# Kernel optimization log

Measured on AMD Instinct MI355X. Metric: run time of the kernel, lower is better.

Reference implementation:

```python
import jax, jax.numpy as jnp
import numpy as np

T_, B_, DIM, NB, D, H_, W_ = 4, 4, 256, 16, 16, 32, 32
VTH_L1_LOW = VTH_L1_HIGH = 0.5
EPS = 1e-5

# ---- surrogate-gradient spike (ATan surrogate, alpha=2.0, spikingjelly default) ----
@jax.custom_vjp
def spike(x):
    return (x >= 0).astype(x.dtype)

def _spk_fwd(x):
    return spike(x), x

def _spk_bwd(x, g):
    a = 2.0
    return (g * (a / 2.0) / (1.0 + (jnp.pi / 2.0 * a * x) ** 2),)

spike.defvjp(_spk_fwd, _spk_bwd)

def lif(x, tau=2.0, vth=1.0):
    # MultiStepLIFNode: v += (x - v)/tau; fire at vth; hard reset (detach_reset)
    def step(v, xt):
        v = v + (xt - v) / tau
        s = spike(v - vth)
        v = v * (1.0 - jax.lax.stop_gradient(s))
        return v, s
    _, s = jax.lax.scan(step, jnp.zeros_like(x[0]), x)
    return s

def haar_mat(n):
    m = np.zeros((n, n), np.float32)
    s = 1.0 / np.sqrt(2.0)
    for i in range(n // 2):
        m[i, 2 * i] = s; m[i, 2 * i + 1] = s          # low-pass rows
        m[n // 2 + i, 2 * i] = s; m[n // 2 + i, 2 * i + 1] = -s  # high-pass rows
    return jnp.asarray(m)

def bn(x, g, b):  # training-mode BatchNorm2d over (N,C,H,W)
    mu = jnp.mean(x, axis=(0, 2, 3), keepdims=True)
    var = jnp.var(x, axis=(0, 2, 3), keepdims=True)
    return g.reshape(1, -1, 1, 1) * (x - mu) * jax.lax.rsqrt(var + EPS) + b.reshape(1, -1, 1, 1)

def conv(x, w, b):
    y = jax.lax.conv_general_dilated(x, w, (1, 1), 'SAME',
                                     dimension_numbers=('NCHW', 'OIHW', 'NCHW'))
    return y + b.reshape(1, -1, 1, 1)

def band_gate(c, vth, tau):
    # coefficient spiking threshold then channel-energy sparsity gate
    c = c * spike(jnp.abs(c) - vth)
    E = jnp.mean(c * c, axis=(-2, -1), keepdims=True)  # per (T,B,C) energy
    return c * (E > tau).astype(c.dtype)

def _forward(x, haar_weight, conv1_w, conv1_b, conv2_w, conv2_b,
             bn_fwd_g, bn_fwd_b, bn_mul_g, bn_mul_b, bn_inv_g, bn_inv_b,
             bn_c1_g, bn_c1_b, bn_c2_g, bn_c2_b):
    T, B, C, H, W = x.shape
    HmW, HmH = haar_mat(W), haar_mat(H)
    Hh, Wh, TB = H // 2, W // 2, T * B
    s = lif(x)
    # ---- level-1 Haar along W ----
    y = jnp.einsum('vw,tbchw->tbchv', HmW, s)
    low, high = y[..., :Wh], y[..., Wh:]
    low = low * spike(jnp.abs(low) - VTH_L1_LOW)
    high = high * spike(jnp.abs(high) - VTH_L1_HIGH)
    l1 = jnp.concatenate([low, high], axis=2)  # (T,B,2C,H,Wh)
    l1 = bn(l1.reshape(TB, 2 * C, H, Wh), bn_fwd_g, bn_fwd_b).reshape(T, B, 2 * C, H, Wh)
    # ---- level-2 Haar along H + per-band sparsity ----
    lo, hi = l1[:, :, :C], l1[:, :, C:]
    zlo = jnp.einsum('vh,tbchw->tbcvw', HmH, lo)
    zhi = jnp.einsum('vh,tbchw->tbcvw', HmH, hi)
    LL = band_gate(zlo[..., :Hh, :], 0.5, 0.01)
    HL = band_gate(zlo[..., Hh:, :], 0.5, 0.02)
    LH = band_gate(zhi[..., :Hh, :], 0.5, 0.02)
    HH = band_gate(zhi[..., Hh:, :], 0.5, 0.05)
    l2 = jnp.concatenate([LL, HL, LH, HH], axis=2)  # (T,B,4C,Hh,Wh)
    l2 = bn(l2.reshape(TB, 4 * C, Hh, Wh), bn_mul_g, bn_mul_b)
    # ---- block-diagonal multiply ----
    h = l2.reshape(TB, NB, 4 * D, Hh, Wh).transpose(0, 3, 4, 1, 2)  # (TB,Hh,Wh,NB,4D)
    parts = [jnp.einsum('thwbd,bdk->thwbk', h[..., i * D:(i + 1) * D], haar_weight)
             for i in range(4)]
    h = jnp.concatenate(parts, axis=-1)
    h = h.reshape(TB, Hh, Wh, 4 * C).transpose(0, 3, 1, 2).reshape(T, B, 4 * C, Hh, Wh)
    # ---- inverse Haar ----
    LLc, HLc, LHc, HHc = h[:, :, :C], h[:, :, C:2 * C], h[:, :, 2 * C:3 * C], h[:, :, 3 * C:]
    lo = jnp.einsum('vh,tbcvw->tbchw', HmH, jnp.concatenate([LLc, HLc], axis=-2))
    hi = jnp.einsum('vh,tbcvw->tbchw', HmH, jnp.concatenate([LHc, HHc], axis=-2))
    rec = jnp.einsum('vw,tbchv->tbchw', HmW, jnp.concatenate([lo, hi], axis=-1))
    rec = bn(rec.reshape(TB, C, H, W), bn_inv_g, bn_inv_b).reshape(T, B, C, H, W)
    # ---- conv residual paths over block channels ----
    xr = s.reshape(TB * NB, D, H, W)
    c1 = bn(conv(xr, conv1_w, conv1_b).reshape(TB, C, H, W), bn_c1_g, bn_c1_b).reshape(T, B, C, H, W)
    c2 = bn(conv(xr, conv2_w, conv2_b).reshape(TB, C, H, W), bn_c2_g, bn_c2_b).reshape(T, B, C, H, W)
    return rec + c1 + c2

def setup_inputs() -> dict:
    key = jax.random.key(0)
    ks = jax.random.split(key, 4)
    return {
        'x': jax.random.normal(ks[0], (T_, B_, DIM, H_, W_), jnp.float32),
        'haar_weight': 0.02 * jax.random.normal(ks[1], (NB, D, D), jnp.float32),
        'conv1_w': 0.1 * jax.random.normal(ks[2], (D, D, 1, 1), jnp.float32),
        'conv1_b': jnp.zeros((D,), jnp.float32),
        'conv2_w': 0.05 * jax.random.normal(ks[3], (D, D, 3, 3), jnp.float32),
        'conv2_b': jnp.zeros((D,), jnp.float32),
        'bn_fwd_g': jnp.ones((2 * DIM,), jnp.float32), 'bn_fwd_b': jnp.zeros((2 * DIM,), jnp.float32),
        'bn_mul_g': jnp.ones((4 * DIM,), jnp.float32), 'bn_mul_b': jnp.zeros((4 * DIM,), jnp.float32),
        'bn_inv_g': jnp.ones((DIM,), jnp.float32), 'bn_inv_b': jnp.zeros((DIM,), jnp.float32),
        'bn_c1_g': jnp.ones((DIM,), jnp.float32), 'bn_c1_b': jnp.zeros((DIM,), jnp.float32),
        'bn_c2_g': jnp.ones((DIM,), jnp.float32), 'bn_c2_b': jnp.zeros((DIM,), jnp.float32),
    }

def reference(x, haar_weight, conv1_w, conv1_b, conv2_w, conv2_b,
              bn_fwd_g, bn_fwd_b, bn_mul_g, bn_mul_b, bn_inv_g, bn_inv_b,
              bn_c1_g, bn_c1_b, bn_c2_g, bn_c2_b):
    return _forward(x, haar_weight, conv1_w, conv1_b, conv2_w, conv2_b,
                    bn_fwd_g, bn_fwd_b, bn_mul_g, bn_mul_b, bn_inv_g, bn_inv_b,
                    bn_c1_g, bn_c1_b, bn_c2_g, bn_c2_b)
```

## Files before the change

### kernel.cpp

```cpp
#include <hip/hip_runtime.h>
#include <hip/hip_bf16.h>

#define T_ 4
#define B_ 4
#define C_ 256
#define H_ 32
#define W_ 32
#define TB_ 16
#define Hh_ 16
#define Wh_ 16
#define INVS2 0.70710678118654752440f
#define EPSBN 1e-5f

#define OFF_HW   0
#define OFF_W1   4096
#define OFF_B1   4352
#define OFF_W2   4368
#define OFF_B2   6672
#define OFF_G1   6688
#define OFF_BE1  7200
#define OFF_G2   7712
#define OFF_BE2  8736
#define OFF_G3   9760
#define OFF_BE3  10016
#define OFF_G4   10272
#define OFF_BE4  10528
#define OFF_G5   10784
#define OFF_BE5  11040
#define W_TOTAL  11296
#define NSUMS    4608

struct WPtrs { const void* p[15]; };

typedef __attribute__((ext_vector_type(8))) short short8;
typedef __attribute__((ext_vector_type(4))) float f32x4;

__device__ inline float bf2f(__hip_bfloat16 v) { return __bfloat162float(v); }
__device__ inline float bfu(unsigned short u) { return __uint_as_float((unsigned)u << 16); }

__global__ __launch_bounds__(256) void k_prep(const unsigned short* __restrict__ xr,
                                              WPtrs wp,
                                              __hip_bfloat16* __restrict__ wc,
                                              float* __restrict__ sums,
                                              int* __restrict__ flag) {
    int tid = threadIdx.x;
    int cnt = 0;
    for (int i = tid; i < 2048; i += 256) {
        int e = (xr[i] >> 7) & 0xFF;
        if (e >= 134) cnt++;
    }
    for (int o = 1; o < 64; o <<= 1) cnt += __shfl_xor(cnt, o, 64);
    __shared__ int sh[4];
    if ((tid & 63) == 0) sh[tid >> 6] = cnt;
    __syncthreads();
    int f = (sh[0] + sh[1] + sh[2] + sh[3] >= 32) ? 1 : 0;
    if (blockIdx.x == 0 && tid == 0) *flag = f;

    const int sizes[15] = {4096, 256, 16, 2304, 16, 512, 512, 1024, 1024,
                           256, 256, 256, 256, 256, 256};
    int i = blockIdx.x * 256 + tid;
    if (i < W_TOTAL) {
        int seg = 0, off = 0;
        while (i >= off + sizes[seg]) { off += sizes[seg]; seg++; }
        int j = i - off;
        float v = f ? ((const float*)wp.p[seg])[j]
                    : bf2f(((const __hip_bfloat16*)wp.p[seg])[j]);
        wc[i] = __float2bfloat16(v);
    }
    if (i < NSUMS) sums[i] = 0.f;
}

__global__ __launch_bounds__(256) void k_lifhaar(const void* __restrict__ x_,
                                                 const int* __restrict__ flag,
                                                 unsigned char* __restrict__ s,
                                                 float* __restrict__ sums1) {
    int bid = blockIdx.x;
    int tid = threadIdx.x;
    int half = bid & 1;
    int c = (bid >> 1) & 255;
    int b = bid >> 9;
    int wp = tid & 15;
    int hl = tid >> 4;
    int h = half * 16 + hl;
    int f = *flag;
    const float* xf = (const float*)x_;
    const unsigned int* xb = (const unsigned int*)x_;
    int n = ((b * 256 + c) * 32 + h) * 32 + 2 * wp;

    float v0 = 0.f, v1 = 0.f;
    float aL = 0.f, qL = 0.f, aH = 0.f, qH = 0.f;
    #pragma unroll
    for (int t = 0; t < T_; ++t) {
        size_t idx = (size_t)t * 1048576 + n;
        float x0, x1;
        if (f) {
            float2 xx = *(const float2*)(xf + idx);
            x0 = xx.x; x1 = xx.y;
        } else {
            unsigned int u = xb[idx >> 1];
            x0 = __uint_as_float(u << 16);
            x1 = __uint_as_float(u & 0xffff0000u);
        }
        v0 += (x0 - v0) * 0.5f;
        v1 += (x1 - v1) * 0.5f;
        float s0 = (v0 >= 1.f) ? 1.f : 0.f;
        float s1 = (v1 >= 1.f) ? 1.f : 0.f;
        v0 *= (1.f - s0);
        v1 *= (1.f - s1);
        int tb = t * 4 + b;
        ((uchar2*)s)[(size_t)(tb * 256 + c) * 512 + h * 16 + wp] =
            make_uchar2((unsigned char)s0, (unsigned char)s1);
        float cl = s0 + s1, ch = s0 - s1;
        aL += cl; qL += cl * cl; aH += ch; qH += ch * ch;
    }
    for (int o = 1; o < 64; o <<= 1) {
        aL += __shfl_xor(aL, o, 64); qL += __shfl_xor(qL, o, 64);
        aH += __shfl_xor(aH, o, 64); qH += __shfl_xor(qH, o, 64);
    }
    __shared__ float part[4][4];
    int lane = tid & 63, wv = tid >> 6;
    if (lane == 0) {
        part[wv][0] = aL; part[wv][1] = qL; part[wv][2] = aH; part[wv][3] = qH;
    }
    __syncthreads();
    if (tid < 4) {
        float tot = part[0][tid] + part[1][tid] + part[2][tid] + part[3][tid];
        const int offs[4] = {0, 512, 256, 768};
        atomicAdd(&sums1[offs[tid] + c], tot);
    }
}

__global__ __launch_bounds__(256) void k_stage2(const unsigned char* __restrict__ s,
                                                const float* __restrict__ sums1,
                                                const __hip_bfloat16* __restrict__ wc,
                                                float* __restrict__ stats,
                                                __hip_bfloat16* __restrict__ l2) {
    int blk = blockIdx.x;
    int c = blk & 255;
    int tb = blk >> 8;
    int tid = threadIdx.x;
    int lane = tid & 63, wv = tid >> 6;

    const float nrm = 1.f / 8192.f;
    float mL = sums1[c] * INVS2 * nrm;
    float vL = fmaxf(sums1[512 + c] * 0.5f * nrm - mL * mL, 0.f);
    float sL = bf2f(wc[OFF_G1 + c]) * rsqrtf(vL + EPSBN);
    float tL = bf2f(wc[OFF_BE1 + c]) - mL * sL;
    float mH = sums1[256 + c] * INVS2 * nrm;
    float vH = fmaxf(sums1[768 + c] * 0.5f * nrm - mH * mH, 0.f);
    float sH = bf2f(wc[OFF_G1 + 256 + c]) * rsqrtf(vH + EPSBN);
    float tH = bf2f(wc[OFF_BE1 + 256 + c]) - mH * sH;
    float slo = sL * INVS2, shi = sH * INVS2;

    int w = tid & 15, v = tid >> 4;
    const uchar2* sp = (const uchar2*)(s + ((size_t)(tb * 256 + c)) * 1024);
    uchar2 pa = sp[(2 * v) * 16 + w];
    uchar2 pb = sp[(2 * v + 1) * 16 + w];
    float lt = (float)(pa.x + pa.y) * slo + tL;
    float lb = (float)(pb.x + pb.y) * slo + tL;
    float ht = (float)((int)pa.x - (int)pa.y) * shi + tH;
    float hb = (float)((int)pb.x - (int)pb.y) * shi + tH;

    float zLL = (lt + lb) * INVS2;
    float zHL = (lt - lb) * INVS2;
    float zLH = (ht + hb) * INVS2;
    float zHH = (ht - hb) * INVS2;
    zLL = (fabsf(zLL) - 0.5f >= 0.f) ? zLL : 0.f;
    zHL = (fabsf(zHL) - 0.5f >= 0.f) ? zHL : 0.f;
    zLH = (fabsf(zLH) - 0.5f >= 0.f) ? zLH : 0.f;
    zHH = (fabsf(zHH) - 0.5f >= 0.f) ? zHH : 0.f;

    float r0 = zLL, r1 = zHL, r2 = zLH, r3 = zHH;
    float q0 = zLL * zLL, q1 = zHL * zHL, q2 = zLH * zLH, q3 = zHH * zHH;
    for (int o = 1; o < 64; o <<= 1) {
        r0 += __shfl_xor(r0, o, 64); r1 += __shfl_xor(r1, o, 64);
        r2 += __shfl_xor(r2, o, 64); r3 += __shfl_xor(r3, o, 64);
        q0 += __shfl_xor(q0, o, 64); q1 += __shfl_xor(q1, o, 64);
        q2 += __shfl_xor(q2, o, 64); q3 += __shfl_xor(q3, o, 64);
    }
    __shared__ float part[4][8];
    if (lane == 0) {
        part[wv][0] = r0; part[wv][1] = r1; part[wv][2] = r2; part[wv][3] = r3;
        part[wv][4] = q0; part[wv][5] = q1; part[wv][6] = q2; part[wv][7] = q3;
    }
    __syncthreads();
    float S0 = part[0][0] + part[1][0] + part[2][0] + part[3][0];
    float S1 = part[0][1] + part[1][1] + part[2][1] + part[3][1];
    float S2 = part[0][2] + part[1][2] + part[2][2] + part[3][2];
    float S3 = part[0][3] + part[1][3] + part[2][3] + part[3][3];
    float Q0 = part[0][4] + part[1][4] + part[2][4] + part[3][4];
    float Q1 = part[0][5] + part[1][5] + part[2][5] + part[3][5];
    float Q2 = part[0][6] + part[1][6] + part[2][6] + part[3][6];
    float Q3 = part[0][7] + part[1][7] + part[2][7] + part[3][7];
    float fLL = (Q0 * (1.f / 256.f) > 0.01f) ? 1.f : 0.f;
    float fHL = (Q1 * (1.f / 256.f) > 0.02f) ? 1.f : 0.f;
    float fLH = (Q2 * (1.f / 256.f) > 0.02f) ? 1.f : 0.f;
    float fHH = (Q3 * (1.f / 256.f) > 0.05f) ? 1.f : 0.f;

    float* sums2 = stats + 1024;
    if (tid < 8) {
        const int cho[8] = {0, 1024, 256, 1280, 512, 1536, 768, 1792};
        const float vals[8] = {fLL * S0, fLL * Q0, fHL * S1, fHL * Q1,
                               fLH * S2, fLH * Q2, fHH * S3, fHH * Q3};
        atomicAdd(&sums2[cho[tid] + c], vals[tid]);
    }

    size_t ob = (((size_t)tb * 1024) + c) * 256 + tid;
    l2[ob]               = __float2bfloat16(zLL * fLL);
    l2[ob + 256u * 256u] = __float2bfloat16(zHL * fHL);
    l2[ob + 512u * 256u] = __float2bfloat16(zLH * fLH);
    l2[ob + 768u * 256u] = __float2bfloat16(zHH * fHH);
}

struct SharedU {
    union {
        struct {
            short lo[1025 * 8];
            short hi[1025 * 8];
            unsigned short w2s[2304];
            unsigned short w1s[256];
            unsigned short bs[32];
            float parts[4][4][16];
        } cv;
        struct {
            float wt[4][16][16];
            float bsc[64], bsh[64];
            float parts2[4][32];
        } mi;
    };
};

__global__ __launch_bounds__(256) void k_convmix(const unsigned char* __restrict__ s,
                                                 const __hip_bfloat16* __restrict__ l2,
                                                 const __hip_bfloat16* __restrict__ wc,
                                                 float* __restrict__ stats,
                                                 __hip_bfloat16* __restrict__ rec,
                                                 __hip_bfloat16* __restrict__ c1,
                                                 __hip_bfloat16* __restrict__ c2) {
    __shared__ SharedU sm;
    int bid = blockIdx.x;
    int tid = threadIdx.x;
    int lane = tid & 63, wv = tid >> 6;

    if (bid < 256) {
        int img = bid;
        const unsigned short* wr = (const unsigned short*)wc;
        for (int i = tid; i < 2304; i += 256) sm.cv.w2s[i] = wr[OFF_W2 + i];
        sm.cv.w1s[tid] = wr[OFF_W1 + tid];
        if (tid < 16) { sm.cv.bs[tid] = wr[OFF_B1 + tid]; sm.cv.bs[16 + tid] = wr[OFF_B2 + tid]; }
        if (tid < 8) {
            ((unsigned int*)sm.cv.lo)[4096 + (tid & 3)] = 0;
            ((unsigned int*)sm.cv.hi)[4096 + (tid & 3)] = 0;
        }
        {
            const unsigned int* sp = (const unsigned int*)(s + (size_t)img * 16384);
            int d2 = tid >> 5;
            int pg = tid & 31;
            unsigned int* dst = (unsigned int*)((d2 < 4) ? sm.cv.lo : sm.cv.hi);
            int dl = d2 & 3;
            #pragma unroll
            for (int p = 0; p < 8; ++p) {
                int base = p * 32 + pg;
                unsigned int u0 = sp[d2 * 512 + base];
                unsigned int u1 = sp[d2 * 512 + 256 + base];
                #pragma unroll
                for (int jj = 0; jj < 4; ++jj) {
                    int j = (jj + pg) & 3;
                    unsigned int b0 = (u0 >> (8 * j)) & 255u;
                    unsigned int b1 = (u1 >> (8 * j)) & 255u;
                    unsigned int val = (b0 ? 0x3F80u : 0u) | ((b1 ? 0x3F80u : 0u) << 16);
                    int pix = p * 128 + pg * 4 + j;
                    dst[pix * 4 + dl] = val;
                }
            }
        }
        __syncthreads();

        int m = lane & 15;
        int g = lane >> 4;
        const int tapA[5] = {0, 2, 4, 6, 8};
        const int tapB[5] = {1, 3, 5, 7, 8};

        short8 afr[5], a1f;
        #pragma unroll
        for (int p = 0; p < 5; ++p) {
            int tap = (g < 2) ? tapA[p] : tapB[p];
            short8 av;
            #pragma unroll
            for (int j = 0; j < 8; ++j) {
                int d = (g & 1) * 8 + j;
                unsigned short w = sm.cv.w2s[m * 144 + d * 9 + tap];
                if (p == 4 && g >= 2) w = 0;
                av[j] = (short)w;
            }
            afr[p] = av;
        }
        #pragma unroll
        for (int j = 0; j < 8; ++j) {
            int d = (g & 1) * 8 + j;
            a1f[j] = (g < 2) ? (short)sm.cv.w1s[m * 16 + d] : (short)0;
        }
        float bias1[4], bias2[4];
        #pragma unroll
        for (int r = 0; r < 4; ++r) {
            bias1[r] = bfu(sm.cv.bs[g * 4 + r]);
            bias2[r] = bfu(sm.cv.bs[16 + g * 4 + r]);
        }

        __hip_bfloat16* o1 = c1 + (size_t)img * 16384;
        __hip_bfloat16* o2 = c2 + (size_t)img * 16384;
        const short* bsrc = (g & 1) ? sm.cv.hi : sm.cv.lo;

        float cs1[4] = {0, 0, 0, 0}, cq1[4] = {0, 0, 0, 0};
        float cs2[4] = {0, 0, 0, 0}, cq2[4] = {0, 0, 0, 0};

        for (int t = wv * 16; t < wv * 16 + 16; ++t) {
            int h = t >> 1;
            int w0 = (t & 1) << 4;
            f32x4 acc2 = {0.f, 0.f, 0.f, 0.f};
            f32x4 acc1 = {0.f, 0.f, 0.f, 0.f};
            #pragma unroll
            for (int p = 0; p < 5; ++p) {
                int tap = (g < 2) ? tapA[p] : tapB[p];
                int row = h + tap / 3 - 1;
                int col = w0 + m + (tap % 3) - 1;
                bool ok = ((unsigned)row < 32u) && ((unsigned)col < 32u);
                int idx = ok ? (row * 32 + col) : 1024;
                short8 bv = *(const short8*)&bsrc[idx * 8];
                acc2 = __builtin_amdgcn_mfma_f32_16x16x32_bf16(afr[p], bv, acc2, 0, 0, 0);
                if (p == 2)
                    acc1 = __builtin_amdgcn_mfma_f32_16x16x32_bf16(a1f, bv, acc1, 0, 0, 0);
            }
            int pix = h * 32 + w0 + m;
            #pragma unroll
            for (int r = 0; r < 4; ++r) {
                int k = g * 4 + r;
                float y1 = acc1[r] + bias1[r];
                float y2 = acc2[r] + bias2[r];
                o1[(size_t)k * 1024 + pix] = __float2bfloat16(y1);
                o2[(size_t)k * 1024 + pix] = __float2bfloat16(y2);
                cs1[r] += y1; cq1[r] += y1 * y1;
                cs2[r] += y2; cq2[r] += y2 * y2;
            }
        }
        #pragma unroll
        for (int o = 1; o < 16; o <<= 1) {
            #pragma unroll
            for (int r = 0; r < 4; ++r) {
                cs1[r] += __shfl_xor(cs1[r], o, 64);
                cq1[r] += __shfl_xor(cq1[r], o, 64);
                cs2[r] += __shfl_xor(cs2[r], o, 64);
                cq2[r] += __shfl_xor(cq2[r], o, 64);
            }
        }
        if (m == 0) {
            #pragma unroll
            for (int r = 0; r < 4; ++r) {
                sm.cv.parts[wv][g][r * 4 + 0] = cs1[r];
                sm.cv.parts[wv][g][r * 4 + 1] = cq1[r];
                sm.cv.parts[wv][g][r * 4 + 2] = cs2[r];
                sm.cv.parts[wv][g][r * 4 + 3] = cq2[r];
            }
        }
        __syncthreads();
        if (tid < 64) {
            int gg = tid >> 4, r = (tid >> 2) & 3, which = tid & 3;
            float tot = sm.cv.parts[0][gg][r * 4 + which] + sm.cv.parts[1][gg][r * 4 + which]
                      + sm.cv.parts[2][gg][r * 4 + which] + sm.cv.parts[3][gg][r * 4 + which];
            int ch = (img & 15) * 16 + gg * 4 + r;
            const int base[4] = {3584, 3840, 4096, 4352};
            atomicAdd(&stats[base[which] + ch], tot);
        }
    } else {
        int mb = bid - 256;
        int cg = mb & 15;
        int tb = mb >> 4;
        const float* sums2 = stats + 1024;

        for (int i = tid; i < 1024; i += 256) {
            int q = i >> 8, rem = i & 255, d = rem >> 4, k = rem & 15;
            int nb = q * 4 + (cg >> 2);
            sm.mi.wt[q][d][k] = bf2f(wc[OFF_HW + nb * 256 + d * 16 + k]);
        }
        if (tid < 64) {
            int q = tid >> 4, d = tid & 15;
            int ch = q * 256 + cg * 16 + d;
            float m = sums2[ch] * (1.f / 4096.f);
            float var = fmaxf(sums2[1024 + ch] * (1.f / 4096.f) - m * m, 0.f);
            float sc = bf2f(wc[OFF_G2 + ch]) * rsqrtf(var + EPSBN);
            sm.mi.bsc[tid] = sc;
            sm.mi.bsh[tid] = bf2f(wc[OFF_BE2 + ch]) - m * sc;
        }
        __syncthreads();

        float h[4][16];
        #pragma unroll
        for (int q = 0; q < 4; ++q)
            #pragma unroll
            for (int k = 0; k < 16; ++k) h[q][k] = 0.f;

        int p = tid;
        #pragma unroll
        for (int q = 0; q < 4; ++q) {
            const __hip_bfloat16* base =
                l2 + ((size_t)tb * 1024 + q * 256 + cg * 16) * 256 + p;
            #pragma unroll
            for (int d = 0; d < 16; ++d) {
                float xv = bf2f(base[d * 256]) * sm.mi.bsc[q * 16 + d] + sm.mi.bsh[q * 16 + d];
                #pragma unroll
                for (int k = 0; k < 16; ++k)
                    h[q][k] = fmaf(xv, sm.mi.wt[q][d][k], h[q][k]);
            }
        }

        int uh = tid >> 4, uw = tid & 15;
        __hip_bfloat16* ob = rec + ((size_t)tb * 256 + cg * 16) * 1024;
        float sk[16], qk[16];
        #pragma unroll
        for (int k = 0; k < 16; ++k) {
            float LL = h[0][k], HL = h[1][k], LH = h[2][k], HH = h[3][k];
            float v00 = 0.5f * (LL + HL + LH + HH);
            float v01 = 0.5f * (LL + HL - LH - HH);
            float v10 = 0.5f * (LL - HL + LH - HH);
            float v11 = 0.5f * (LL - HL - LH + HH);
            __hip_bfloat162 top, bot;
            top.x = __float2bfloat16(v00); top.y = __float2bfloat16(v01);
            bot.x = __float2bfloat16(v10); bot.y = __float2bfloat16(v11);
            *(__hip_bfloat162*)(ob + (size_t)k * 1024 + (2 * uh) * 32 + 2 * uw) = top;
            *(__hip_bfloat162*)(ob + (size_t)k * 1024 + (2 * uh + 1) * 32 + 2 * uw) = bot;
            sk[k] = v00 + v01 + v10 + v11;
            qk[k] = v00 * v00 + v01 * v01 + v10 * v10 + v11 * v11;
        }
        for (int o = 1; o < 64; o <<= 1) {
            #pragma unroll
            for (int k = 0; k < 16; ++k) {
                sk[k] += __shfl_xor(sk[k], o, 64);
                qk[k] += __shfl_xor(qk[k], o, 64);
            }
        }
        if (lane == 0) {
            #pragma unroll
            for (int k = 0; k < 16; ++k) {
                sm.mi.parts2[wv][k * 2]     = sk[k];
                sm.mi.parts2[wv][k * 2 + 1] = qk[k];
            }
        }
        __syncthreads();
        if (tid < 32) {
            int k = tid >> 1, which = tid & 1;
            float tot = sm.mi.parts2[0][tid] + sm.mi.parts2[1][tid]
                      + sm.mi.parts2[2][tid] + sm.mi.parts2[3][tid];
            atomicAdd(&stats[3072 + which * 256 + cg * 16 + k], tot);
        }
    }
}

__global__ __launch_bounds__(256) void k_final(const __hip_bfloat16* __restrict__ rec,
                                               const __hip_bfloat16* __restrict__ c1,
                                               const __hip_bfloat16* __restrict__ c2,
                                               const float* __restrict__ stats,
                                               const __hip_bfloat16* __restrict__ wc,
                                               const int* __restrict__ flag,
                                               void* __restrict__ out_) {
    int n8 = blockIdx.x * 256 + threadIdx.x;
    int c = ((n8 * 8) >> 10) & 255;
    const float inv = 1.f / 16384.f;
    float m3 = stats[3072 + c] * inv;
    float v3 = fmaxf(stats[3328 + c] * inv - m3 * m3, 0.f);
    float sc3 = bf2f(wc[OFF_G3 + c]) * rsqrtf(v3 + EPSBN);
    float sh3 = bf2f(wc[OFF_BE3 + c]) - m3 * sc3;
    float m4 = stats[3584 + c] * inv;
    float v4 = fmaxf(stats[3840 + c] * inv - m4 * m4, 0.f);
    float sc4 = bf2f(wc[OFF_G4 + c]) * rsqrtf(v4 + EPSBN);
    float sh4 = bf2f(wc[OFF_BE4 + c]) - m4 * sc4;
    float m5 = stats[4096 + c] * inv;
    float v5 = fmaxf(stats[4352 + c] * inv - m5 * m5, 0.f);
    float sc5 = bf2f(wc[OFF_G5 + c]) * rsqrtf(v5 + EPSBN);
    float sh5 = bf2f(wc[OFF_BE5 + c]) - m5 * sc5;

    short8 r = ((const short8*)rec)[n8];
    short8 a = ((const short8*)c1)[n8];
    short8 b = ((const short8*)c2)[n8];
    float v[8];
    #pragma unroll
    for (int j = 0; j < 8; ++j) {
        v[j] = bfu((unsigned short)r[j]) * sc3 + sh3
             + bfu((unsigned short)a[j]) * sc4 + sh4
             + bfu((unsigned short)b[j]) * sc5 + sh5;
    }
    if (*flag) {
        float4* o = (float4*)out_;
        o[n8 * 2]     = make_float4(v[0], v[1], v[2], v[3]);
        o[n8 * 2 + 1] = make_float4(v[4], v[5], v[6], v[7]);
    } else {
        short8 o;
        #pragma unroll
        for (int j = 0; j < 8; ++j)
            o[j] = (short)__bfloat16_as_ushort(__float2bfloat16(v[j]));
        ((short8*)out_)[n8] = o;
    }
}

extern "C" void kernel_launch(void* const* d_in, const int* in_sizes, int n_in,
                              void* d_out, int out_size, void* d_ws, size_t ws_size,
                              hipStream_t stream) {
    char* ws = (char*)d_ws;
    unsigned char* s_u8  = (unsigned char*)ws;
    __hip_bfloat16* l2   = (__hip_bfloat16*)(ws + ((size_t)8 << 20));
    __hip_bfloat16* rec  = (__hip_bfloat16*)(ws + ((size_t)16 << 20));
    __hip_bfloat16* c1   = (__hip_bfloat16*)(ws + ((size_t)24 << 20));
    __hip_bfloat16* c2   = (__hip_bfloat16*)(ws + ((size_t)32 << 20));
    __hip_bfloat16* wc   = (__hip_bfloat16*)(ws + ((size_t)40 << 20));
    float* stats         = (float*)(ws + ((size_t)40 << 20) + (64 << 10));
    int* flag            = (int*)(ws + ((size_t)40 << 20) + (128 << 10));

    WPtrs wp;
    for (int i = 0; i < 15; ++i) wp.p[i] = d_in[i + 1];

    dim3 blk(256);
    k_prep<<<dim3(45), blk, 0, stream>>>((const unsigned short*)d_in[0], wp, wc, stats, flag);
    k_lifhaar<<<dim3(2048), blk, 0, stream>>>(d_in[0], flag, s_u8, stats);
    k_stage2<<<dim3(4096), blk, 0, stream>>>(s_u8, stats, wc, stats, l2);
    k_convmix<<<dim3(512), blk, 0, stream>>>(s_u8, l2, wc, stats, rec, c1, c2);
    k_final<<<dim3(2048), blk, 0, stream>>>(rec, c1, c2, stats, wc, flag, d_out);
}
```

Before: 150.8 us.

## Fuse four stage kernels into one persistent kernel with software grid barriers

Merges the LIF/Haar, stage-2 band gating, conv-mix and final BN-sum kernels into one 512-block persistent kernel. Phases are separated by an atomic-counter grid barrier with hierarchical counters, and the per-block work from the old larger grids is folded into loops. This removes the launch gaps and tail effects between kernels. In exchange it requires all 512 blocks to be co-resident (launch_bounds 256,2), serializes work per block, and adds spin-wait barrier overhead.

Measured after the change: 302.4 us. 2.01x slower.

```diff
diff --git a/kernel.cpp b/kernel.cpp
--- a/kernel.cpp
+++ b/kernel.cpp
@@ -11,6 +11,7 @@
 #define Wh_ 16
 #define INVS2 0.70710678118654752440f
 #define EPSBN 1e-5f
+#define NBLK 512
 
 #define OFF_HW   0
 #define OFF_W1   4096
@@ -38,10 +39,11 @@
 __device__ inline float bf2f(__hip_bfloat16 v) { return __bfloat162float(v); }
 __device__ inline float bfu(unsigned short u) { return __uint_as_float((unsigned)u << 16); }
 
-__global__ __launch_bounds__(256) void k_prep(const unsigned short* __restrict__ xr,
+__global__ __launch_bounds__(256) void k_init(const unsigned short* __restrict__ xr,
                                               WPtrs wp,
                                               __hip_bfloat16* __restrict__ wc,
                                               float* __restrict__ sums,
+                                              int* __restrict__ bar,
                                               int* __restrict__ flag) {
     int tid = threadIdx.x;
     int cnt = 0;
@@ -68,151 +70,25 @@
         wc[i] = __float2bfloat16(v);
     }
     if (i < NSUMS) sums[i] = 0.f;
+    if (i < 16) bar[i] = 0;
 }
 
-__global__ __launch_bounds__(256) void k_lifhaar(const void* __restrict__ x_,
-                                                 const int* __restrict__ flag,
-                                                 unsigned char* __restrict__ s,
-                                                 float* __restrict__ sums1) {
-    int bid = blockIdx.x;
-    int tid = threadIdx.x;
-    int half = bid & 1;
-    int c = (bid >> 1) & 255;
-    int b = bid >> 9;
-    int wp = tid & 15;
-    int hl = tid >> 4;
-    int h = half * 16 + hl;
-    int f = *flag;
-    const float* xf = (const float*)x_;
-    const unsigned int* xb = (const unsigned int*)x_;
-    int n = ((b * 256 + c) * 32 + h) * 32 + 2 * wp;
-
-    float v0 = 0.f, v1 = 0.f;
-    float aL = 0.f, qL = 0.f, aH = 0.f, qH = 0.f;
-    #pragma unroll
-    for (int t = 0; t < T_; ++t) {
-        size_t idx = (size_t)t * 1048576 + n;
-        float x0, x1;
-        if (f) {
-            float2 xx = *(const float2*)(xf + idx);
-            x0 = xx.x; x1 = xx.y;
-        } else {
-            unsigned int u = xb[idx >> 1];
-            x0 = __uint_as_float(u << 16);
-            x1 = __uint_as_float(u & 0xffff0000u);
-        }
-        v0 += (x0 - v0) * 0.5f;
-        v1 += (x1 - v1) * 0.5f;
-        float s0 = (v0 >= 1.f) ? 1.f : 0.f;
-        float s1 = (v1 >= 1.f) ? 1.f : 0.f;
-        v0 *= (1.f - s0);
-        v1 *= (1.f - s1);
-        int tb = t * 4 + b;
-        ((uchar2*)s)[(size_t)(tb * 256 + c) * 512 + h * 16 + wp] =
-            make_uchar2((unsigned char)s0, (unsigned char)s1);
-        float cl = s0 + s1, ch = s0 - s1;
-        aL += cl; qL += cl * cl; aH += ch; qH += ch * ch;
-    }
-    for (int o = 1; o < 64; o <<= 1) {
-        aL += __shfl_xor(aL, o, 64); qL += __shfl_xor(qL, o, 64);
-        aH += __shfl_xor(aH, o, 64); qH += __shfl_xor(qH, o, 64);
-    }
-    __shared__ float part[4][4];
-    int lane = tid & 63, wv = tid >> 6;
-    if (lane == 0) {
-        part[wv][0] = aL; part[wv][1] = qL; part[wv][2] = aH; part[wv][3] = qH;
-    }
+__device__ __forceinline__ void gbar(int* bs, int phase) {
     __syncthreads();
-    if (tid < 4) {
-        float tot = part[0][tid] + part[1][tid] + part[2][tid] + part[3][tid];
-        const int offs[4] = {0, 512, 256, 768};
-        atomicAdd(&sums1[offs[tid] + c], tot);
-    }
+    if (threadIdx.x == 0) {
+        __threadfence();
+        int t = atomicAdd(&bs[2 + (blockIdx.x & 7)], 1) + 1;
+        if (t == phase * (NBLK / 8)) {
+            int m = atomicAdd(&bs[1], 1) + 1;
+            if (m == phase * 8) atomicAdd(&bs[0], 1);
+        }
+        while (atomicAdd(&bs[0], 0) < phase) __builtin_amdgcn_s_sleep(2);
+        __threadfence();
+    }
+    __syncthreads();
 }
 
-__global__ __launch_bounds__(256) void k_stage2(const unsigned char* __restrict__ s,
-                                                const float* __restrict__ sums1,
-                                                const __hip_bfloat16* __restrict__ wc,
-                                                float* __restrict__ stats,
-                                                __hip_bfloat16* __restrict__ l2) {
-    int blk = blockIdx.x;
-    int c = blk & 255;
-    int tb = blk >> 8;
-    int tid = threadIdx.x;
-    int lane = tid & 63, wv = tid >> 6;
-
-    const float nrm = 1.f / 8192.f;
-    float mL = sums1[c] * INVS2 * nrm;
-    float vL = fmaxf(sums1[512 + c] * 0.5f * nrm - mL * mL, 0.f);
-    float sL = bf2f(wc[OFF_G1 + c]) * rsqrtf(vL + EPSBN);
-    float tL = bf2f(wc[OFF_BE1 + c]) - mL * sL;
-    float mH = sums1[256 + c] * INVS2 * nrm;
-    float vH = fmaxf(sums1[768 + c] * 0.5f * nrm - mH * mH, 0.f);
-    float sH = bf2f(wc[OFF_G1 + 256 + c]) * rsqrtf(vH + EPSBN);
-    float tH = bf2f(wc[OFF_BE1 + 256 + c]) - mH * sH;
-    float slo = sL * INVS2, shi = sH * INVS2;
-
-    int w = tid & 15, v = tid >> 4;
-    const uchar2* sp = (const uchar2*)(s + ((size_t)(tb * 256 + c)) * 1024);
-    uchar2 pa = sp[(2 * v) * 16 + w];
-    uchar2 pb = sp[(2 * v + 1) * 16 + w];
-    float lt = (float)(pa.x + pa.y) * slo + tL;
-    float lb = (float)(pb.x + pb.y) * slo + tL;
-    float ht = (float)((int)pa.x - (int)pa.y) * shi + tH;
-    float hb = (float)((int)pb.x - (int)pb.y) * shi + tH;
-
-    float zLL = (lt + lb) * INVS2;
-    float zHL = (lt - lb) * INVS2;
-    float zLH = (ht + hb) * INVS2;
-    float zHH = (ht - hb) * INVS2;
-    zLL = (fabsf(zLL) - 0.5f >= 0.f) ? zLL : 0.f;
-    zHL = (fabsf(zHL) - 0.5f >= 0.f) ? zHL : 0.f;
-    zLH = (fabsf(zLH) - 0.5f >= 0.f) ? zLH : 0.f;
-    zHH = (fabsf(zHH) - 0.5f >= 0.f) ? zHH : 0.f;
-
-    float r0 = zLL, r1 = zHL, r2 = zLH, r3 = zHH;
-    float q0 = zLL * zLL, q1 = zHL * zHL, q2 = zLH * zLH, q3 = zHH * zHH;
-    for (int o = 1; o < 64; o <<= 1) {
-        r0 += __shfl_xor(r0, o, 64); r1 += __shfl_xor(r1, o, 64);
-        r2 += __shfl_xor(r2, o, 64); r3 += __shfl_xor(r3, o, 64);
-        q0 += __shfl_xor(q0, o, 64); q1 += __shfl_xor(q1, o, 64);
-        q2 += __shfl_xor(q2, o, 64); q3 += __shfl_xor(q3, o, 64);
-    }
-    __shared__ float part[4][8];
-    if (lane == 0) {
-        part[wv][0] = r0; part[wv][1] = r1; part[wv][2] = r2; part[wv][3] = r3;
-        part[wv][4] = q0; part[wv][5] = q1; part[wv][6] = q2; part[wv][7] = q3;
-    }
-    __syncthreads();
-    float S0 = part[0][0] + part[1][0] + part[2][0] + part[3][0];
-    float S1 = part[0][1] + part[1][1] + part[2][1] + part[3][1];
-    float S2 = part[0][2] + part[1][2] + part[2][2] + part[3][2];
-    float S3 = part[0][3] + part[1][3] + part[2][3] + part[3][3];
-    float Q0 = part[0][4] + part[1][4] + part[2][4] + part[3][4];
-    float Q1 = part[0][5] + part[1][5] + part[2][5] + part[3][5];
-    float Q2 = part[0][6] + part[1][6] + part[2][6] + part[3][6];
-    float Q3 = part[0][7] + part[1][7] + part[2][7] + part[3][7];
-    float fLL = (Q0 * (1.f / 256.f) > 0.01f) ? 1.f : 0.f;
-    float fHL = (Q1 * (1.f / 256.f) > 0.02f) ? 1.f : 0.f;
-    float fLH = (Q2 * (1.f / 256.f) > 0.02f) ? 1.f : 0.f;
-    float fHH = (Q3 * (1.f / 256.f) > 0.05f) ? 1.f : 0.f;
-
-    float* sums2 = stats + 1024;
-    if (tid < 8) {
-        const int cho[8] = {0, 1024, 256, 1280, 512, 1536, 768, 1792};
-        const float vals[8] = {fLL * S0, fLL * Q0, fHL * S1, fHL * Q1,
-                               fLH * S2, fLH * Q2, fHH * S3, fHH * Q3};
-        atomicAdd(&sums2[cho[tid] + c], vals[tid]);
-    }
-
-    size_t ob = (((size_t)tb * 1024) + c) * 256 + tid;
-    l2[ob]               = __float2bfloat16(zLL * fLL);
-    l2[ob + 256u * 256u] = __float2bfloat16(zHL * fHL);
-    l2[ob + 512u * 256u] = __float2bfloat16(zLH * fLH);
-    l2[ob + 768u * 256u] = __float2bfloat16(zHH * fHH);
-}
-
-struct SharedU {
+struct SM {
     union {
         struct {
             short lo[1025 * 8];
@@ -227,20 +103,160 @@
             float bsc[64], bsh[64];
             float parts2[4][32];
         } mi;
+        float p48[4][8];
     };
 };
 
-__global__ __launch_bounds__(256) void k_convmix(const unsigned char* __restrict__ s,
-                                                 const __hip_bfloat16* __restrict__ l2,
-                                                 const __hip_bfloat16* __restrict__ wc,
-                                                 float* __restrict__ stats,
-                                                 __hip_bfloat16* __restrict__ rec,
-                                                 __hip_bfloat16* __restrict__ c1,
-                                                 __hip_bfloat16* __restrict__ c2) {
-    __shared__ SharedU sm;
+__global__ __launch_bounds__(256, 2) void k_fused(const void* __restrict__ x_,
+                                                  const __hip_bfloat16* __restrict__ wc,
+                                                  float* __restrict__ stats,
+                                                  int* __restrict__ bar,
+                                                  const int* __restrict__ flag,
+                                                  unsigned char* __restrict__ s,
+                                                  __hip_bfloat16* __restrict__ l2,
+                                                  __hip_bfloat16* __restrict__ rec,
+                                                  __hip_bfloat16* __restrict__ c1,
+                                                  __hip_bfloat16* __restrict__ c2,
+                                                  void* __restrict__ out_) {
+    __shared__ SM sm;
     int bid = blockIdx.x;
     int tid = threadIdx.x;
     int lane = tid & 63, wv = tid >> 6;
+    int f = *flag;
+
+    {
+        const float* xf = (const float*)x_;
+        const unsigned int* xb = (const unsigned int*)x_;
+        for (int u = bid * 4; u < bid * 4 + 4; ++u) {
+            int half = u & 1;
+            int c = (u >> 1) & 255;
+            int b = u >> 9;
+            int wp = tid & 15;
+            int h = half * 16 + (tid >> 4);
+            int n = ((b * 256 + c) * 32 + h) * 32 + 2 * wp;
+
+            float v0 = 0.f, v1 = 0.f;
+            float aL = 0.f, qL = 0.f, aH = 0.f, qH = 0.f;
+            #pragma unroll
+            for (int t = 0; t < T_; ++t) {
+                size_t idx = (size_t)t * 1048576 + n;
+                float x0, x1;
+                if (f) {
+                    float2 xx = *(const float2*)(xf + idx);
+                    x0 = xx.x; x1 = xx.y;
+                } else {
+                    unsigned int uu = xb[idx >> 1];
+                    x0 = __uint_as_float(uu << 16);
+                    x1 = __uint_as_float(uu & 0xffff0000u);
+                }
+                v0 += (x0 - v0) * 0.5f;
+                v1 += (x1 - v1) * 0.5f;
+                float s0 = (v0 >= 1.f) ? 1.f : 0.f;
+                float s1 = (v1 >= 1.f) ? 1.f : 0.f;
+                v0 *= (1.f - s0);
+                v1 *= (1.f - s1);
+                int tb = t * 4 + b;
+                ((uchar2*)s)[(size_t)(tb * 256 + c) * 512 + h * 16 + wp] =
+                    make_uchar2((unsigned char)s0, (unsigned char)s1);
+                float cl = s0 + s1, ch = s0 - s1;
+                aL += cl; qL += cl * cl; aH += ch; qH += ch * ch;
+            }
+            for (int o = 1; o < 64; o <<= 1) {
+                aL += __shfl_xor(aL, o, 64); qL += __shfl_xor(qL, o, 64);
+                aH += __shfl_xor(aH, o, 64); qH += __shfl_xor(qH, o, 64);
+            }
+            if (lane == 0) {
+                sm.p48[wv][0] = aL; sm.p48[wv][1] = qL;
+                sm.p48[wv][2] = aH; sm.p48[wv][3] = qH;
+            }
+            __syncthreads();
+            if (tid < 4) {
+                float tot = sm.p48[0][tid] + sm.p48[1][tid] + sm.p48[2][tid] + sm.p48[3][tid];
+                const int offs[4] = {0, 512, 256, 768};
+                atomicAdd(&stats[offs[tid] + c], tot);
+            }
+            __syncthreads();
+        }
+    }
+    gbar(bar, 1);
+
+    {
+        float* sums2 = stats + 1024;
+        for (int u = bid * 8; u < bid * 8 + 8; ++u) {
+            int c = u & 255;
+            int tb = u >> 8;
+
+            const float nrm = 1.f / 8192.f;
+            float mL = stats[c] * INVS2 * nrm;
+            float vL = fmaxf(stats[512 + c] * 0.5f * nrm - mL * mL, 0.f);
+            float sL = bf2f(wc[OFF_G1 + c]) * rsqrtf(vL + EPSBN);
+            float tL = bf2f(wc[OFF_BE1 + c]) - mL * sL;
+            float mH = stats[256 + c] * INVS2 * nrm;
+            float vH = fmaxf(stats[768 + c] * 0.5f * nrm - mH * mH, 0.f);
+            float sH = bf2f(wc[OFF_G1 + 256 + c]) * rsqrtf(vH + EPSBN);
+            float tH = bf2f(wc[OFF_BE1 + 256 + c]) - mH * sH;
+            float slo = sL * INVS2, shi = sH * INVS2;
+
+            int w = tid & 15, v = tid >> 4;
+            const uchar2* sp = (const uchar2*)(s + ((size_t)(tb * 256 + c)) * 1024);
+            uchar2 pa = sp[(2 * v) * 16 + w];
+            uchar2 pb = sp[(2 * v + 1) * 16 + w];
+            float lt = (float)(pa.x + pa.y) * slo + tL;
+            float lb = (float)(pb.x + pb.y) * slo + tL;
+            float ht = (float)((int)pa.x - (int)pa.y) * shi + tH;
+            float hb = (float)((int)pb.x - (int)pb.y) * shi + tH;
+
+            float zLL = (lt + lb) * INVS2;
+            float zHL = (lt - lb) * INVS2;
+            float zLH = (ht + hb) * INVS2;
+            float zHH = (ht - hb) * INVS2;
+            zLL = (fabsf(zLL) - 0.5f >= 0.f) ? zLL : 0.f;
+            zHL = (fabsf(zHL) - 0.5f >= 0.f) ? zHL : 0.f;
+            zLH = (fabsf(zLH) - 0.5f >= 0.f) ? zLH : 0.f;
+            zHH = (fabsf(zHH) - 0.5f >= 0.f) ? zHH : 0.f;
+
+            float r0 = zLL, r1 = zHL, r2 = zLH, r3 = zHH;
+            float q0 = zLL * zLL, q1 = zHL * zHL, q2 = zLH * zLH, q3 = zHH * zHH;
+            for (int o = 1; o < 64; o <<= 1) {
+                r0 += __shfl_xor(r0, o, 64); r1 += __shfl_xor(r1, o, 64);
+                r2 += __shfl_xor(r2, o, 64); r3 += __shfl_xor(r3, o, 64);
+                q0 += __shfl_xor(q0, o, 64); q1 += __shfl_xor(q1, o, 64);
+                q2 += __shfl_xor(q2, o, 64); q3 += __shfl_xor(q3, o, 64);
+            }
+            if (lane == 0) {
+                sm.p48[wv][0] = r0; sm.p48[wv][1] = r1; sm.p48[wv][2] = r2; sm.p48[wv][3] = r3;
+                sm.p48[wv][4] = q0; sm.p48[wv][5] = q1; sm.p48[wv][6] = q2; sm.p48[wv][7] = q3;
+            }
+            __syncthreads();
+            float S0 = sm.p48[0][0] + sm.p48[1][0] + sm.p48[2][0] + sm.p48[3][0];
+            float S1 = sm.p48[0][1] + sm.p48[1][1] + sm.p48[2][1] + sm.p48[3][1];
+            float S2 = sm.p48[0][2] + sm.p48[1][2] + sm.p48[2][2] + sm.p48[3][2];
+            float S3 = sm.p48[0][3] + sm.p48[1][3] + sm.p48[2][3] + sm.p48[3][3];
+            float Q0 = sm.p48[0][4] + sm.p48[1][4] + sm.p48[2][4] + sm.p48[3][4];
+            float Q1 = sm.p48[0][5] + sm.p48[1][5] + sm.p48[2][5] + sm.p48[3][5];
+            float Q2 = sm.p48[0][6] + sm.p48[1][6] + sm.p48[2][6] + sm.p48[3][6];
+            float Q3 = sm.p48[0][7] + sm.p48[1][7] + sm.p48[2][7] + sm.p48[3][7];
+            float fLL = (Q0 * (1.f / 256.f) > 0.01f) ? 1.f : 0.f;
+            float fHL = (Q1 * (1.f / 256.f) > 0.02f) ? 1.f : 0.f;
+            float fLH = (Q2 * (1.f / 256.f) > 0.02f) ? 1.f : 0.f;
+            float fHH = (Q3 * (1.f / 256.f) > 0.05f) ? 1.f : 0.f;
+
+            if (tid < 8) {
+                const int cho[8] = {0, 1024, 256, 1280, 512, 1536, 768, 1792};
+                const float vals[8] = {fLL * S0, fLL * Q0, fHL * S1, fHL * Q1,
+                                       fLH * S2, fLH * Q2, fHH * S3, fHH * Q3};
+                atomicAdd(&sums2[cho[tid] + c], vals[tid]);
+            }
+
+            size_t ob = (((size_t)tb * 1024) + c) * 256 + tid;
+            l2[ob]               = __float2bfloat16(zLL * fLL);
+            l2[ob + 256u * 256u] = __float2bfloat16(zHL * fHL);
+            l2[ob + 512u * 256u] = __float2bfloat16(zLH * fLH);
+            l2[ob + 768u * 256u] = __float2bfloat16(zHH * fHH);
+            __syncthreads();
+        }
+    }
+    gbar(bar, 2);
 
     if (bid < 256) {
         int img = bid;
@@ -453,51 +469,49 @@
             atomicAdd(&stats[3072 + which * 256 + cg * 16 + k], tot);
         }
     }
-}
-
-__global__ __launch_bounds__(256) void k_final(const __hip_bfloat16* __restrict__ rec,
-                                               const __hip_bfloat16* __restrict__ c1,
-                                               const __hip_bfloat16* __restrict__ c2,
-                                               const float* __restrict__ stats,
-                                               const __hip_bfloat16* __restrict__ wc,
-                                               const int* __restrict__ flag,
-                                               void* __restrict__ out_) {
-    int n8 = blockIdx.x * 256 + threadIdx.x;
-    int c = ((n8 * 8) >> 10) & 255;
-    const float inv = 1.f / 16384.f;
-    float m3 = stats[3072 + c] * inv;
-    float v3 = fmaxf(stats[3328 + c] * inv - m3 * m3, 0.f);
-    float sc3 = bf2f(wc[OFF_G3 + c]) * rsqrtf(v3 + EPSBN);
-    float sh3 = bf2f(wc[OFF_BE3 + c]) - m3 * sc3;
-    float m4 = stats[3584 + c] * inv;
-    float v4 = fmaxf(stats[3840 + c] * inv - m4 * m4, 0.f);
-    float sc4 = bf2f(wc[OFF_G4 + c]) * rsqrtf(v4 + EPSBN);
-    float sh4 = bf2f(wc[OFF_BE4 + c]) - m4 * sc4;
-    float m5 = stats[4096 + c] * inv;
-    float v5 = fmaxf(stats[4352 + c] * inv - m5 * m5, 0.f);
-    float sc5 = bf2f(wc[OFF_G5 + c]) * rsqrtf(v5 + EPSBN);
-    float sh5 = bf2f(wc[OFF_BE5 + c]) - m5 * sc5;
-
-    short8 r = ((const short8*)rec)[n8];
-    short8 a = ((const short8*)c1)[n8];
-    short8 b = ((const short8*)c2)[n8];
-    float v[8];
-    #pragma unroll
-    for (int j = 0; j < 8; ++j) {
-        v[j] = bfu((unsigned short)r[j]) * sc3 + sh3
-             + bfu((unsigned short)a[j]) * sc4 + sh4
-             + bfu((unsigned short)b[j]) * sc5 + sh5;
-    }
-    if (*flag) {
-        float4* o = (float4*)out_;
-        o[n8 * 2]     = make_float4(v[0], v[1], v[2], v[3]);
-        o[n8 * 2 + 1] = make_float4(v[4], v[5], v[6], v[7]);
-    } else {
-        short8 o;
-        #pragma unroll
-        for (int j = 0; j < 8; ++j)
-            o[j] = (short)__bfloat16_as_ushort(__float2bfloat16(v[j]));
-        ((short8*)out_)[n8] = o;
+    gbar(bar, 3);
+
+    {
+        const float inv = 1.f / 16384.f;
+        #pragma unroll
+        for (int i = 0; i < 4; ++i) {
+            int n8 = bid * 1024 + i * 256 + tid;
+            int c = ((n8 * 8) >> 10) & 255;
+            float m3 = stats[3072 + c] * inv;
+            float v3 = fmaxf(stats[3328 + c] * inv - m3 * m3, 0.f);
+            float sc3 = bf2f(wc[OFF_G3 + c]) * rsqrtf(v3 + EPSBN);
+            float sh3 = bf2f(wc[OFF_BE3 + c]) - m3 * sc3;
+            float m4 = stats[3584 + c] * inv;
+            float v4 = fmaxf(stats[3840 + c] * inv - m4 * m4, 0.f);
+            float sc4 = bf2f(wc[OFF_G4 + c]) * rsqrtf(v4 + EPSBN);
+            float sh4 = bf2f(wc[OFF_BE4 + c]) - m4 * sc4;
+            float m5 = stats[4096 + c] * inv;
+            float v5 = fmaxf(stats[4352 + c] * inv - m5 * m5, 0.f);
+            float sc5 = bf2f(wc[OFF_G5 + c]) * rsqrtf(v5 + EPSBN);
+            float sh5 = bf2f(wc[OFF_BE5 + c]) - m5 * sc5;
+
+            short8 r = ((const short8*)rec)[n8];
+            short8 a = ((const short8*)c1)[n8];
+            short8 b = ((const short8*)c2)[n8];
+            float v[8];
+            #pragma unroll
+            for (int j = 0; j < 8; ++j) {
+                v[j] = bfu((unsigned short)r[j]) * sc3 + sh3
+                     + bfu((unsigned short)a[j]) * sc4 + sh4
+                     + bfu((unsigned short)b[j]) * sc5 + sh5;
+            }
+            if (f) {
+                float4* o = (float4*)out_;
+                o[n8 * 2]     = make_float4(v[0], v[1], v[2], v[3]);
+                o[n8 * 2 + 1] = make_float4(v[4], v[5], v[6], v[7]);
+            } else {
+                short8 o;
+                #pragma unroll
+                for (int j = 0; j < 8; ++j)
+                    o[j] = (short)__bfloat16_as_ushort(__float2bfloat16(v[j]));
+                ((short8*)out_)[n8] = o;
+            }
+        }
     }
 }
 
@@ -513,14 +527,13 @@
     __hip_bfloat16* wc   = (__hip_bfloat16*)(ws + ((size_t)40 << 20));
     float* stats         = (float*)(ws + ((size_t)40 << 20) + (64 << 10));
     int* flag            = (int*)(ws + ((size_t)40 << 20) + (128 << 10));
+    int* bar             = (int*)(ws + ((size_t)40 << 20) + (132 << 10));
 
     WPtrs wp;
     for (int i = 0; i < 15; ++i) wp.p[i] = d_in[i + 1];
 
     dim3 blk(256);
-    k_prep<<<dim3(45), blk, 0, stream>>>((const unsigned short*)d_in[0], wp, wc, stats, flag);
-    k_lifhaar<<<dim3(2048), blk, 0, stream>>>(d_in[0], flag, s_u8, stats);
-    k_stage2<<<dim3(4096), blk, 0, stream>>>(s_u8, stats, wc, stats, l2);
-    k_convmix<<<dim3(512), blk, 0, stream>>>(s_u8, l2, wc, stats, rec, c1, c2);
-    k_final<<<dim3(2048), blk, 0, stream>>>(rec, c1, c2, stats, wc, flag, d_out);
+    k_init<<<dim3(45), blk, 0, stream>>>((const unsigned short*)d_in[0], wp, wc, stats, bar, flag);
+    k_fused<<<dim3(NBLK), blk, 0, stream>>>(d_in[0], wc, stats, bar, flag,
+                                            s_u8, l2, rec, c1, c2, d_out);
 }
```
